# Performance work log

Hardware: AMD Instinct MI355X
Metric: run time of the kernel (lower is better)

The kernel has to match this reference:

```python
import jax, jax.numpy as jnp
import numpy as np

B, S, C, H = 256, 512, 64, 128  # batch, seq_len, input channels, LSTM hidden


def setup_inputs() -> dict:
    key = jax.random.key(0)
    ks = jax.random.split(key, 9)
    s = 1.0 / np.sqrt(H)  # torch nn.LSTM init: U(-1/sqrt(H), 1/sqrt(H))
    u = lambda k, shape: jax.random.uniform(k, shape, jnp.float32, -s, s)
    return {
        "x": jax.random.normal(ks[0], (B, S, C), jnp.float32),
        # layer 0 (input size C)
        "Wih0": u(ks[1], (4 * H, C)),
        "Whh0": u(ks[2], (4 * H, H)),
        "bih0": u(ks[3], (4 * H,)),
        "bhh0": u(ks[4], (4 * H,)),
        # layer 1 (input size H)
        "Wih1": u(ks[5], (4 * H, H)),
        "Whh1": u(ks[6], (4 * H, H)),
        "bih1": u(ks[7], (4 * H,)),
        "bhh1": u(ks[8], (4 * H,)),
    }


def _lstm_layer(x, Wih, Whh, bih, bhh):
    """x: (S, B, in) -> outputs h_t for all t: (S, B, H). Torch gate order i,f,g,o."""
    Hh = Whh.shape[1]
    # Input-to-hidden GEMM hoisted out of the recurrence (batched over S).
    xg = jnp.einsum('sbc,gc->sbg', x, Wih) + bih + bhh  # (S, B, 4H)

    def step(carry, xt):
        h, c = carry
        g = xt + h @ Whh.T  # (B, 4H)
        i, f, gg, o = jnp.split(g, 4, axis=-1)
        i = jax.nn.sigmoid(i)
        f = jax.nn.sigmoid(f)
        gg = jnp.tanh(gg)
        o = jax.nn.sigmoid(o)
        c = f * c + i * gg
        h = o * jnp.tanh(c)
        return (h, c), h

    h0 = jnp.zeros((x.shape[1], Hh), x.dtype)
    _, ys = jax.lax.scan(step, (h0, h0), xg)
    return ys


def reference(x, Wih0, Whh0, bih0, bhh0, Wih1, Whh1, bih1, bhh1):
    xs = jnp.transpose(x, (1, 0, 2))  # (B,S,C) -> (S,B,C), matching x.permute(1,0,2)
    y1 = _lstm_layer(xs, Wih0, Whh0, bih0, bhh0)
    y2 = _lstm_layer(y1, Wih1, Whh1, bih1, bhh1)
    return y2[-1]  # x[-1, :, :]: last timestep of top layer, (B, H)
```

## Files before the change

### kernel.cpp

```cpp
#include <hip/hip_runtime.h>
#include <cstdint>
#include <cstddef>


#define S_LEN 512
#define B_SZ  256
#define C_IN  64
#define HDIM  128
#define CH    16
#define NBLK  32

using short8  = __attribute__((ext_vector_type(8))) short;
using float4v = __attribute__((ext_vector_type(4))) float;

__device__ __forceinline__ unsigned short f2b(float f) {
    union { float f; unsigned int u; } v; v.f = f;
    unsigned int u = v.u;
    return (unsigned short)((u + 0x7FFFu + ((u >> 16) & 1u)) >> 16);
}
__device__ __forceinline__ float sig_(float x) {
    return __builtin_amdgcn_rcpf(1.0f + __builtin_amdgcn_exp2f(x * -1.442695041f));
}
__device__ __forceinline__ float tanh_(float x) {
    return 1.0f - 2.0f * __builtin_amdgcn_rcpf(1.0f + __builtin_amdgcn_exp2f(x * 2.885390082f));
}

__global__ void prep_kernel(const float* __restrict__ x,
                            const float* __restrict__ wih0, const float* __restrict__ whh0,
                            const float* __restrict__ bih0, const float* __restrict__ bhh0,
                            const float* __restrict__ wih1, const float* __restrict__ whh1,
                            const float* __restrict__ bih1, const float* __restrict__ bhh1,
                            unsigned short* __restrict__ whh0_b, unsigned short* __restrict__ wih0_b,
                            unsigned short* __restrict__ whh1_b, unsigned short* __restrict__ wih1_b,
                            float* __restrict__ bias0, float* __restrict__ bias1,
                            unsigned short* __restrict__ xb) {
    int i = blockIdx.x * blockDim.x + threadIdx.x;
    if (i < B_SZ * S_LEN * C_IN) xb[i] = f2b(x[i]);
    if (i < 4 * HDIM * HDIM) {
        whh0_b[i] = f2b(whh0[i]);
        whh1_b[i] = f2b(whh1[i]);
        wih1_b[i] = f2b(wih1[i]);
    }
    if (i < 4 * HDIM * C_IN) wih0_b[i] = f2b(wih0[i]);
    if (i < 4 * HDIM) {
        bias0[i] = bih0[i] + bhh0[i];
        bias1[i] = bih1[i] + bhh1[i];
    }
}

template<int KIN, bool IS_L0>
__device__ __forceinline__ void lstm_layer(
    unsigned short* hbuf,
    const unsigned short* __restrict__ in_seq,
    const unsigned short* __restrict__ wih_b,
    const unsigned short* __restrict__ whh_b,
    const float* __restrict__ bias,
    unsigned short* __restrict__ y1,
    float* __restrict__ final_out,
    int* __restrict__ flags, int blk) {
    constexpr int NKIN = KIN / 32;
    const int tid = threadIdx.x;
    const int w = tid >> 6, L = tid & 63, q = L >> 4, r = L & 15;
    const int boff = blk * 8, j0 = w * 16;
    const int rowload = (r >> 2) * 2 + (r & 1);

    short8 whh[4][4], wih[4][NKIN];
    float bias_s[4];
#pragma unroll
    for (int g = 0; g < 4; ++g) {
        const int nrow = g * HDIM + j0 + r;
#pragma unroll
        for (int kk = 0; kk < 4; ++kk)
            whh[g][kk] = *(const short8*)(whh_b + (size_t)nrow * HDIM + kk * 32 + q * 8);
#pragma unroll
        for (int kk = 0; kk < NKIN; ++kk)
            wih[g][kk] = *(const short8*)(wih_b + (size_t)nrow * KIN + kk * 32 + q * 8);
        bias_s[g] = bias[g * HDIM + j0 + r];
    }

    for (int idx = tid; idx < 2 * 2048; idx += 512) hbuf[idx] = 0;
    float cf[2] = {0.f, 0.f};

    const unsigned short* p;
    size_t stride;
    if constexpr (IS_L0) {
        p = in_seq + ((size_t)(boff + rowload) * S_LEN) * C_IN + q * 8;
        stride = C_IN;
    } else {
        p = in_seq + (size_t)(boff + rowload) * HDIM + q * 8;
        stride = (size_t)B_SZ * HDIM;
    }

    if constexpr (!IS_L0) {
        if (tid == 0)
            while (__hip_atomic_load(flags + blk * 32, __ATOMIC_ACQUIRE,
                                     __HIP_MEMORY_SCOPE_AGENT) != 1)
                __builtin_amdgcn_s_sleep(8);
    }
    __syncthreads();

    short8 xA[NKIN], xB[NKIN];
#pragma unroll
    for (int kk = 0; kk < NKIN; ++kk) xA[kk] = *(const short8*)(p + kk * 32);
    p += stride;

    const int cc = tid & 15, ii = (tid & 127) >> 4;
    const int mii = 4 * (ii >> 1) + (ii & 1);
    unsigned short* yst = y1 + (size_t)(boff + ii) * HDIM + cc * 8;

    const int j = j0 + r;
    const int chunkbase = (j >> 3) * 128 + (j & 7);
    float* fout = final_out ? final_out + (size_t)(boff + 2 * q) * HDIM + j : nullptr;

    auto step = [&](unsigned short* cur, unsigned short* nxt, short8* xc, short8* xn, int t) {
        short8 hfrag[4];
#pragma unroll
        for (int kk = 0; kk < 4; ++kk)
            hfrag[kk] = *(const short8*)(cur + ((kk * 4 + q) * 16 + r) * 8);

        if (t < S_LEN - 1) {
            if constexpr (!IS_L0) {
                if (((t + 1) & (CH - 1)) == 0) {
                    const int ch = (t + 1) / CH;
                    if (tid == 0)
                        while (__hip_atomic_load(flags + blk * 32 + ch, __ATOMIC_ACQUIRE,
                                                 __HIP_MEMORY_SCOPE_AGENT) != ch + 1)
                            __builtin_amdgcn_s_sleep(8);
                    __syncthreads();
                }
            }
#pragma unroll
            for (int kk = 0; kk < NKIN; ++kk) xn[kk] = *(const short8*)(p + kk * 32);
        }
        p += stride;

        float4v acc[4];
#pragma unroll
        for (int g = 0; g < 4; ++g) {
            float4v a = {bias_s[g], bias_s[g], bias_s[g], bias_s[g]};
#pragma unroll
            for (int kk = 0; kk < 4; ++kk)
                a = __builtin_amdgcn_mfma_f32_16x16x32_bf16(hfrag[kk], whh[g][kk], a, 0, 0, 0);
#pragma unroll
            for (int kk = 0; kk < NKIN; ++kk)
                a = __builtin_amdgcn_mfma_f32_16x16x32_bf16(xc[kk], wih[g][kk], a, 0, 0, 0);
            acc[g] = a;
        }

#pragma unroll
        for (int rr = 0; rr < 2; ++rr) {
            const float iv = sig_(acc[0][rr]);
            const float fv = sig_(acc[1][rr]);
            const float gv = tanh_(acc[2][rr]);
            const float ov = sig_(acc[3][rr]);
            cf[rr] = fv * cf[rr] + iv * gv;
            const float hv = ov * tanh_(cf[rr]);
            nxt[chunkbase + (4 * q + rr) * 8] = f2b(hv);
            if constexpr (!IS_L0) {
                if (t == S_LEN - 1) fout[rr * HDIM] = hv;
            }
        }
        __syncthreads();

        if constexpr (IS_L0) {
            if (tid < 128)
                *(short8*)yst = *(const short8*)(nxt + cc * 128 + mii * 8);
            yst += (size_t)B_SZ * HDIM;
            if ((t & (CH - 1)) == (CH - 1)) {
                __threadfence();
                __syncthreads();
                if (tid == 0) {
                    const int ch = t / CH;
                    __hip_atomic_store(flags + blk * 32 + ch, ch + 1, __ATOMIC_RELEASE,
                                       __HIP_MEMORY_SCOPE_AGENT);
                }
            }
        }
    };

    unsigned short* b0 = hbuf;
    unsigned short* b1 = hbuf + 2048;
    for (int t = 0; t < S_LEN; t += 2) {
        step(b0, b1, xA, xB, t);
        step(b1, b0, xB, xA, t + 1);
    }
}

__global__ __launch_bounds__(512, 2)
void lstm_pipe(const unsigned short* __restrict__ xb,
               const unsigned short* __restrict__ wih0_b, const unsigned short* __restrict__ whh0_b,
               const float* __restrict__ bias0,
               const unsigned short* __restrict__ wih1_b, const unsigned short* __restrict__ whh1_b,
               const float* __restrict__ bias1,
               unsigned short* __restrict__ y1, float* __restrict__ out,
               int* __restrict__ flags) {
    __shared__ __align__(16) unsigned short hbuf[2 * 2048];
    if (blockIdx.x < NBLK)
        lstm_layer<C_IN, true>(hbuf, xb, wih0_b, whh0_b, bias0, y1, nullptr, flags, blockIdx.x);
    else
        lstm_layer<HDIM, false>(hbuf, y1, wih1_b, whh1_b, bias1, nullptr, out, flags,
                                blockIdx.x - NBLK);
}


extern "C" void kernel_launch(void* const* d_in, const int* in_sizes, int n_in,
                              void* d_out, int out_size, void* d_ws, size_t ws_size,
                              hipStream_t stream) {
    const float* x    = (const float*)d_in[0];
    const float* wih0 = (const float*)d_in[1];
    const float* whh0 = (const float*)d_in[2];
    const float* bih0 = (const float*)d_in[3];
    const float* bhh0 = (const float*)d_in[4];
    const float* wih1 = (const float*)d_in[5];
    const float* whh1 = (const float*)d_in[6];
    const float* bih1 = (const float*)d_in[7];
    const float* bhh1 = (const float*)d_in[8];

    char* ws = (char*)d_ws;
    unsigned short* whh0_b = (unsigned short*)(ws + 0);
    unsigned short* wih0_b = (unsigned short*)(ws + 131072);
    unsigned short* whh1_b = (unsigned short*)(ws + 196608);
    unsigned short* wih1_b = (unsigned short*)(ws + 327680);
    float*          bias0  = (float*)(ws + 458752);
    float*          bias1  = (float*)(ws + 460800);
    int*            flags  = (int*)(ws + 462848);
    unsigned short* xb     = (unsigned short*)(ws + 524288);
    unsigned short* y1     = (unsigned short*)(ws + 17301504);

    hipMemsetAsync(flags, 0, 4096, stream);

    prep_kernel<<<(B_SZ * S_LEN * C_IN + 255) / 256, 256, 0, stream>>>(
        x, wih0, whh0, bih0, bhh0, wih1, whh1, bih1, bhh1,
        whh0_b, wih0_b, whh1_b, wih1_b, bias0, bias1, xb);

    lstm_pipe<<<dim3(2 * NBLK), dim3(512), 0, stream>>>(
        xb, wih0_b, whh0_b, bias0, wih1_b, whh1_b, bias1, y1, (float*)d_out, flags);
}
```

Baseline: 734.0 us.

## Fuse both LSTM layers into one wavefront-skewed kernel with precomputed layer-0 input gates

Replaces the two-layer flag-synchronized pipeline (64 blocks, layer-1 blocks polling global flags on chunks of layer-0 output) with a single kernel where each block runs both layers. Layer 1 lags layer 0 by one step, so both recurrences share one barrier per step and the layer-1 input comes straight from shared memory. The layer-0 input projection moves into a separate parallel GEMM kernel that stores bf16 gate preactivations, and the per-step barrier becomes a raw s_waitcnt plus s_barrier. This removes the global y1 round trip, the flag polling and the x bf16 conversion pass. In exchange each block does twice the MFMA work per step on only 32 blocks, holds three weight sets in registers, and adds bf16 rounding of the input-gate preactivations.

```diff
diff --git a/kernel.cpp b/kernel.cpp
--- a/kernel.cpp
+++ b/kernel.cpp
@@ -7,199 +7,231 @@
 #define B_SZ  256
 #define C_IN  64
 #define HDIM  128
-#define CH    16
-#define NBLK  32
+#define XG_TSTRIDE (32 * 512 * 8)
 
 using short8  = __attribute__((ext_vector_type(8))) short;
 using float4v = __attribute__((ext_vector_type(4))) float;
+
+template<bool V> struct Flag { static constexpr bool value = V; };
 
 __device__ __forceinline__ unsigned short f2b(float f) {
     union { float f; unsigned int u; } v; v.f = f;
     unsigned int u = v.u;
     return (unsigned short)((u + 0x7FFFu + ((u >> 16) & 1u)) >> 16);
 }
+__device__ __forceinline__ float b2f(unsigned short s) {
+    union { unsigned int u; float f; } v; v.u = ((unsigned int)s) << 16;
+    return v.f;
+}
 __device__ __forceinline__ float sig_(float x) {
     return __builtin_amdgcn_rcpf(1.0f + __builtin_amdgcn_exp2f(x * -1.442695041f));
 }
 __device__ __forceinline__ float tanh_(float x) {
     return 1.0f - 2.0f * __builtin_amdgcn_rcpf(1.0f + __builtin_amdgcn_exp2f(x * 2.885390082f));
 }
-
-__global__ void prep_kernel(const float* __restrict__ x,
-                            const float* __restrict__ wih0, const float* __restrict__ whh0,
-                            const float* __restrict__ bih0, const float* __restrict__ bhh0,
+__device__ __forceinline__ short8 load8_f2b(const float* s) {
+    const float4v f0 = *(const float4v*)s;
+    const float4v f1 = *(const float4v*)(s + 4);
+    short8 t;
+#pragma unroll
+    for (int e = 0; e < 4; ++e) {
+        t[e]     = (short)f2b(f0[e]);
+        t[e + 4] = (short)f2b(f1[e]);
+    }
+    return t;
+}
+
+__global__ void conv_kernel(const float* __restrict__ whh0,
                             const float* __restrict__ wih1, const float* __restrict__ whh1,
                             const float* __restrict__ bih1, const float* __restrict__ bhh1,
-                            unsigned short* __restrict__ whh0_b, unsigned short* __restrict__ wih0_b,
-                            unsigned short* __restrict__ whh1_b, unsigned short* __restrict__ wih1_b,
-                            float* __restrict__ bias0, float* __restrict__ bias1,
-                            unsigned short* __restrict__ xb) {
+                            unsigned short* __restrict__ whh0_b, unsigned short* __restrict__ wih1_b,
+                            unsigned short* __restrict__ whh1_b, float* __restrict__ bias1) {
     int i = blockIdx.x * blockDim.x + threadIdx.x;
-    if (i < B_SZ * S_LEN * C_IN) xb[i] = f2b(x[i]);
     if (i < 4 * HDIM * HDIM) {
         whh0_b[i] = f2b(whh0[i]);
+        wih1_b[i] = f2b(wih1[i]);
         whh1_b[i] = f2b(whh1[i]);
-        wih1_b[i] = f2b(wih1[i]);
-    }
-    if (i < 4 * HDIM * C_IN) wih0_b[i] = f2b(wih0[i]);
-    if (i < 4 * HDIM) {
-        bias0[i] = bih0[i] + bhh0[i];
-        bias1[i] = bih1[i] + bhh1[i];
-    }
-}
-
-template<int KIN, bool IS_L0>
-__device__ __forceinline__ void lstm_layer(
-    unsigned short* hbuf,
-    const unsigned short* __restrict__ in_seq,
-    const unsigned short* __restrict__ wih_b,
-    const unsigned short* __restrict__ whh_b,
-    const float* __restrict__ bias,
-    unsigned short* __restrict__ y1,
-    float* __restrict__ final_out,
-    int* __restrict__ flags, int blk) {
-    constexpr int NKIN = KIN / 32;
+    }
+    if (i < 4 * HDIM) bias1[i] = bih1[i] + bhh1[i];
+}
+
+__global__ __launch_bounds__(512, 2)
+void xg_gemm(const float* __restrict__ x, const float* __restrict__ wih0,
+             const float* __restrict__ bih0, const float* __restrict__ bhh0,
+             unsigned short* __restrict__ xg) {
     const int tid = threadIdx.x;
     const int w = tid >> 6, L = tid & 63, q = L >> 4, r = L & 15;
-    const int boff = blk * 8, j0 = w * 16;
+    const int blk = blockIdx.x, tch = blockIdx.y;
+    const int boff = blk * 8, j = w * 16 + r;
     const int rowload = (r >> 2) * 2 + (r & 1);
 
-    short8 whh[4][4], wih[4][NKIN];
-    float bias_s[4];
+    short8 wf[4][2]; float bias_s[4];
 #pragma unroll
     for (int g = 0; g < 4; ++g) {
-        const int nrow = g * HDIM + j0 + r;
-#pragma unroll
-        for (int kk = 0; kk < 4; ++kk)
-            whh[g][kk] = *(const short8*)(whh_b + (size_t)nrow * HDIM + kk * 32 + q * 8);
-#pragma unroll
-        for (int kk = 0; kk < NKIN; ++kk)
-            wih[g][kk] = *(const short8*)(wih_b + (size_t)nrow * KIN + kk * 32 + q * 8);
-        bias_s[g] = bias[g * HDIM + j0 + r];
-    }
-
-    for (int idx = tid; idx < 2 * 2048; idx += 512) hbuf[idx] = 0;
-    float cf[2] = {0.f, 0.f};
-
-    const unsigned short* p;
-    size_t stride;
-    if constexpr (IS_L0) {
-        p = in_seq + ((size_t)(boff + rowload) * S_LEN) * C_IN + q * 8;
-        stride = C_IN;
-    } else {
-        p = in_seq + (size_t)(boff + rowload) * HDIM + q * 8;
-        stride = (size_t)B_SZ * HDIM;
-    }
-
-    if constexpr (!IS_L0) {
-        if (tid == 0)
-            while (__hip_atomic_load(flags + blk * 32, __ATOMIC_ACQUIRE,
-                                     __HIP_MEMORY_SCOPE_AGENT) != 1)
-                __builtin_amdgcn_s_sleep(8);
-    }
+        const int nrow = g * HDIM + j;
+#pragma unroll
+        for (int kk = 0; kk < 2; ++kk)
+            wf[g][kk] = load8_f2b(wih0 + (size_t)nrow * C_IN + kk * 32 + q * 8);
+        bias_s[g] = bih0[nrow] + bhh0[nrow];
+    }
+
+    const float* px = x + ((size_t)(boff + rowload) * S_LEN + (size_t)tch * 32) * C_IN + q * 8;
+    unsigned short* po = xg + ((size_t)(tch * 32) * 32 + blk) * 4096 + (size_t)tid * 8;
+
+    for (int tt = 0; tt < 32; ++tt) {
+        short8 xa[2];
+#pragma unroll
+        for (int kk = 0; kk < 2; ++kk) xa[kk] = load8_f2b(px + kk * 32);
+        float4v a[4];
+#pragma unroll
+        for (int g = 0; g < 4; ++g) a[g] = (float4v){bias_s[g], bias_s[g], 0.f, 0.f};
+#pragma unroll
+        for (int kk = 0; kk < 2; ++kk)
+#pragma unroll
+            for (int g = 0; g < 4; ++g)
+                a[g] = __builtin_amdgcn_mfma_f32_16x16x32_bf16(xa[kk], wf[g][kk], a[g], 0, 0, 0);
+        short8 o;
+#pragma unroll
+        for (int g = 0; g < 4; ++g) {
+            o[2 * g]     = (short)f2b(a[g][0]);
+            o[2 * g + 1] = (short)f2b(a[g][1]);
+        }
+        *(short8*)po = o;
+        px += C_IN;
+        po += XG_TSTRIDE;
+    }
+}
+
+__global__ __launch_bounds__(512, 2)
+void lstm_fused(const unsigned short* __restrict__ whh0_b,
+                const unsigned short* __restrict__ wih1_b,
+                const unsigned short* __restrict__ whh1_b,
+                const float* __restrict__ bias1,
+                const unsigned short* __restrict__ xg,
+                float* __restrict__ out) {
+    __shared__ __align__(16) unsigned short hbuf[4 * 2048];
+    const int tid = threadIdx.x;
+    const int w = tid >> 6, L = tid & 63, q = L >> 4, r = L & 15;
+    const int blk = blockIdx.x;
+    const int boff = blk * 8, j = w * 16 + r;
+
+    short8 whh0[4][4], wih1[4][4], whh1[4][4];
+    float b1s[4];
+#pragma unroll
+    for (int g = 0; g < 4; ++g) {
+        const size_t nrow = (size_t)(g * HDIM + j);
+#pragma unroll
+        for (int kk = 0; kk < 4; ++kk) {
+            whh0[g][kk] = *(const short8*)(whh0_b + nrow * HDIM + kk * 32 + q * 8);
+            wih1[g][kk] = *(const short8*)(wih1_b + nrow * HDIM + kk * 32 + q * 8);
+            whh1[g][kk] = *(const short8*)(whh1_b + nrow * HDIM + kk * 32 + q * 8);
+        }
+        b1s[g] = bias1[g * HDIM + j];
+    }
+
+    for (int idx = tid; idx < 4 * 1024; idx += 512) ((unsigned int*)hbuf)[idx] = 0u;
+
+    float cf0[2] = {0.f, 0.f}, cf1[2] = {0.f, 0.f};
+    const int chunkbase = (j >> 3) * 128 + (j & 7);
+    const int rdoff = q * 128 + r * 8;
+    float* fout = out + (size_t)(boff + 2 * q) * HDIM + j;
+
+    const unsigned short* pxg = xg + (size_t)blk * 4096 + (size_t)tid * 8;
+    short8 xgA = *(const short8*)pxg;
+    pxg += XG_TSTRIDE;
+    short8 xgB;
+
     __syncthreads();
 
-    short8 xA[NKIN], xB[NKIN];
-#pragma unroll
-    for (int kk = 0; kk < NKIN; ++kk) xA[kk] = *(const short8*)(p + kk * 32);
-    p += stride;
-
-    const int cc = tid & 15, ii = (tid & 127) >> 4;
-    const int mii = 4 * (ii >> 1) + (ii & 1);
-    unsigned short* yst = y1 + (size_t)(boff + ii) * HDIM + cc * 8;
-
-    const int j = j0 + r;
-    const int chunkbase = (j >> 3) * 128 + (j & 7);
-    float* fout = final_out ? final_out + (size_t)(boff + 2 * q) * HDIM + j : nullptr;
-
-    auto step = [&](unsigned short* cur, unsigned short* nxt, short8* xc, short8* xn, int t) {
-        short8 hfrag[4];
-#pragma unroll
-        for (int kk = 0; kk < 4; ++kk)
-            hfrag[kk] = *(const short8*)(cur + ((kk * 4 + q) * 16 + r) * 8);
-
-        if (t < S_LEN - 1) {
-            if constexpr (!IS_L0) {
-                if (((t + 1) & (CH - 1)) == 0) {
-                    const int ch = (t + 1) / CH;
-                    if (tid == 0)
-                        while (__hip_atomic_load(flags + blk * 32 + ch, __ATOMIC_ACQUIRE,
-                                                 __HIP_MEMORY_SCOPE_AGENT) != ch + 1)
-                            __builtin_amdgcn_s_sleep(8);
-                    __syncthreads();
-                }
+    auto step = [&](auto D0_, auto D1_, auto FIN_,
+                    unsigned short* r0, unsigned short* w0,
+                    unsigned short* r1, unsigned short* w1,
+                    short8& xc, short8& xn) {
+        constexpr bool D0  = decltype(D0_)::value;
+        constexpr bool D1  = decltype(D1_)::value;
+        constexpr bool FIN = decltype(FIN_)::value;
+
+        if constexpr (!FIN) {
+            xn = *(const short8*)pxg;
+            pxg += XG_TSTRIDE;
+        }
+
+        float4v a0[4], a1[4];
+        if constexpr (D0) {
+#pragma unroll
+            for (int g = 0; g < 4; ++g)
+                a0[g] = (float4v){b2f((unsigned short)xc[2 * g]),
+                                  b2f((unsigned short)xc[2 * g + 1]), 0.f, 0.f};
+        }
+        if constexpr (D1) {
+#pragma unroll
+            for (int g = 0; g < 4; ++g) a1[g] = (float4v){b1s[g], b1s[g], 0.f, 0.f};
+        }
+
+#pragma unroll
+        for (int kk = 0; kk < 4; ++kk) {
+            const short8 h0f = *(const short8*)(r0 + kk * 512 + rdoff);
+            if constexpr (D0)
+#pragma unroll
+                for (int g = 0; g < 4; ++g)
+                    a0[g] = __builtin_amdgcn_mfma_f32_16x16x32_bf16(h0f, whh0[g][kk], a0[g], 0, 0, 0);
+            if constexpr (D1)
+#pragma unroll
+                for (int g = 0; g < 4; ++g)
+                    a1[g] = __builtin_amdgcn_mfma_f32_16x16x32_bf16(h0f, wih1[g][kk], a1[g], 0, 0, 0);
+        }
+
+        if constexpr (D0) {
+#pragma unroll
+            for (int rr = 0; rr < 2; ++rr) {
+                const float iv = sig_(a0[0][rr]);
+                const float fv = sig_(a0[1][rr]);
+                const float gv = tanh_(a0[2][rr]);
+                const float ov = sig_(a0[3][rr]);
+                cf0[rr] = fv * cf0[rr] + iv * gv;
+                w0[chunkbase + (4 * q + rr) * 8] = f2b(ov * tanh_(cf0[rr]));
             }
-#pragma unroll
-            for (int kk = 0; kk < NKIN; ++kk) xn[kk] = *(const short8*)(p + kk * 32);
-        }
-        p += stride;
-
-        float4v acc[4];
-#pragma unroll
-        for (int g = 0; g < 4; ++g) {
-            float4v a = {bias_s[g], bias_s[g], bias_s[g], bias_s[g]};
-#pragma unroll
-            for (int kk = 0; kk < 4; ++kk)
-                a = __builtin_amdgcn_mfma_f32_16x16x32_bf16(hfrag[kk], whh[g][kk], a, 0, 0, 0);
-#pragma unroll
-            for (int kk = 0; kk < NKIN; ++kk)
-                a = __builtin_amdgcn_mfma_f32_16x16x32_bf16(xc[kk], wih[g][kk], a, 0, 0, 0);
-            acc[g] = a;
-        }
-
-#pragma unroll
-        for (int rr = 0; rr < 2; ++rr) {
-            const float iv = sig_(acc[0][rr]);
-            const float fv = sig_(acc[1][rr]);
-            const float gv = tanh_(acc[2][rr]);
-            const float ov = sig_(acc[3][rr]);
-            cf[rr] = fv * cf[rr] + iv * gv;
-            const float hv = ov * tanh_(cf[rr]);
-            nxt[chunkbase + (4 * q + rr) * 8] = f2b(hv);
-            if constexpr (!IS_L0) {
-                if (t == S_LEN - 1) fout[rr * HDIM] = hv;
+        }
+
+        if constexpr (D1) {
+#pragma unroll
+            for (int kk = 0; kk < 4; ++kk) {
+                const short8 h1f = *(const short8*)(r1 + kk * 512 + rdoff);
+#pragma unroll
+                for (int g = 0; g < 4; ++g)
+                    a1[g] = __builtin_amdgcn_mfma_f32_16x16x32_bf16(h1f, whh1[g][kk], a1[g], 0, 0, 0);
             }
-        }
-        __syncthreads();
-
-        if constexpr (IS_L0) {
-            if (tid < 128)
-                *(short8*)yst = *(const short8*)(nxt + cc * 128 + mii * 8);
-            yst += (size_t)B_SZ * HDIM;
-            if ((t & (CH - 1)) == (CH - 1)) {
-                __threadfence();
-                __syncthreads();
-                if (tid == 0) {
-                    const int ch = t / CH;
-                    __hip_atomic_store(flags + blk * 32 + ch, ch + 1, __ATOMIC_RELEASE,
-                                       __HIP_MEMORY_SCOPE_AGENT);
-                }
+#pragma unroll
+            for (int rr = 0; rr < 2; ++rr) {
+                const float iv = sig_(a1[0][rr]);
+                const float fv = sig_(a1[1][rr]);
+                const float gv = tanh_(a1[2][rr]);
+                const float ov = sig_(a1[3][rr]);
+                cf1[rr] = fv * cf1[rr] + iv * gv;
+                const float hv = ov * tanh_(cf1[rr]);
+                if constexpr (FIN) fout[rr * HDIM] = hv;
+                else w1[chunkbase + (4 * q + rr) * 8] = f2b(hv);
             }
         }
+
+        if constexpr (!FIN)
+            asm volatile("s_waitcnt lgkmcnt(0)\n\ts_barrier" ::: "memory");
     };
 
-    unsigned short* b0 = hbuf;
-    unsigned short* b1 = hbuf + 2048;
-    for (int t = 0; t < S_LEN; t += 2) {
-        step(b0, b1, xA, xB, t);
-        step(b1, b0, xB, xA, t + 1);
-    }
-}
-
-__global__ __launch_bounds__(512, 2)
-void lstm_pipe(const unsigned short* __restrict__ xb,
-               const unsigned short* __restrict__ wih0_b, const unsigned short* __restrict__ whh0_b,
-               const float* __restrict__ bias0,
-               const unsigned short* __restrict__ wih1_b, const unsigned short* __restrict__ whh1_b,
-               const float* __restrict__ bias1,
-               unsigned short* __restrict__ y1, float* __restrict__ out,
-               int* __restrict__ flags) {
-    __shared__ __align__(16) unsigned short hbuf[2 * 2048];
-    if (blockIdx.x < NBLK)
-        lstm_layer<C_IN, true>(hbuf, xb, wih0_b, whh0_b, bias0, y1, nullptr, flags, blockIdx.x);
-    else
-        lstm_layer<HDIM, false>(hbuf, y1, wih1_b, whh1_b, bias1, nullptr, out, flags,
-                                blockIdx.x - NBLK);
+    unsigned short* h0A = hbuf;
+    unsigned short* h0B = hbuf + 2048;
+    unsigned short* h1A = hbuf + 4096;
+    unsigned short* h1B = hbuf + 6144;
+    using T = Flag<true>; using F = Flag<false>;
+
+    step(T{}, F{}, F{}, h0A, h0B, h1A, h1B, xgA, xgB);
+#pragma unroll 1
+    for (int k = 0; k < 255; ++k) {
+        step(T{}, T{}, F{}, h0B, h0A, h1B, h1A, xgB, xgA);
+        step(T{}, T{}, F{}, h0A, h0B, h1A, h1B, xgA, xgB);
+    }
+    step(T{}, T{}, F{}, h0B, h0A, h1B, h1A, xgB, xgA);
+    step(F{}, T{}, T{}, h0A, h0B, h1A, h1B, xgA, xgB);
 }
 
 
@@ -218,21 +250,14 @@
 
     char* ws = (char*)d_ws;
     unsigned short* whh0_b = (unsigned short*)(ws + 0);
-    unsigned short* wih0_b = (unsigned short*)(ws + 131072);
-    unsigned short* whh1_b = (unsigned short*)(ws + 196608);
-    unsigned short* wih1_b = (unsigned short*)(ws + 327680);
-    float*          bias0  = (float*)(ws + 458752);
-    float*          bias1  = (float*)(ws + 460800);
-    int*            flags  = (int*)(ws + 462848);
-    unsigned short* xb     = (unsigned short*)(ws + 524288);
-    unsigned short* y1     = (unsigned short*)(ws + 17301504);
-
-    hipMemsetAsync(flags, 0, 4096, stream);
-
-    prep_kernel<<<(B_SZ * S_LEN * C_IN + 255) / 256, 256, 0, stream>>>(
-        x, wih0, whh0, bih0, bhh0, wih1, whh1, bih1, bhh1,
-        whh0_b, wih0_b, whh1_b, wih1_b, bias0, bias1, xb);
-
-    lstm_pipe<<<dim3(2 * NBLK), dim3(512), 0, stream>>>(
-        xb, wih0_b, whh0_b, bias0, wih1_b, whh1_b, bias1, y1, (float*)d_out, flags);
-}
+    unsigned short* wih1_b = (unsigned short*)(ws + 131072);
+    unsigned short* whh1_b = (unsigned short*)(ws + 262144);
+    float*          bias1  = (float*)(ws + 393216);
+    unsigned short* xgp    = (unsigned short*)(ws + 524288);
+
+    conv_kernel<<<256, 256, 0, stream>>>(whh0, wih1, whh1, bih1, bhh1,
+                                         whh0_b, wih1_b, whh1_b, bias1);
+    xg_gemm<<<dim3(32, 16), 512, 0, stream>>>(x, wih0, bih0, bhh0, xgp);
+    lstm_fused<<<32, 512, 0, stream>>>(whh0_b, wih1_b, whh1_b, bias1, xgp,
+                                       (float*)d_out);
+}
```

Measured after the change: 1.076 ms. 46.5% more time.
